# Kernel optimization log

Measured on AMD Instinct MI355X. Metric: run time of the kernel, lower is better.

The kernel has to match this reference:

```python
import jax, jax.numpy as jnp
import numpy as np

NUM_LAYERS = 6
D_MODEL = 256
N_HEADS = 8
N_LEVELS = 4
N_POINTS = 4
D_FFN = 1024
HEAD_DIM = D_MODEL // N_HEADS
B = 2
NQ = 1600
SPATIAL = np.array([[64, 64], [32, 32], [16, 16], [8, 8]], dtype=np.int64)  # (H_l, W_l)
LEVEL_START = np.concatenate([[0], np.cumsum(SPATIAL.prod(1))[:-1]]).astype(np.int64)
S_TOTAL = int(SPATIAL.prod(1).sum())  # 5440


def layer_norm(x, g, b, eps=1e-5):
    mu = x.mean(-1, keepdims=True)
    var = ((x - mu) ** 2).mean(-1, keepdims=True)
    return (x - mu) * jax.lax.rsqrt(var + eps) * g + b


def mha(q, k, v, wq, bq, wk, bk, wv, bv, wo, bo):
    # torch nn.MultiheadAttention math (dropout=eval identity)
    Bb, N, d = q.shape
    def proj(x, w, bias):
        return (x @ w.T + bias).reshape(Bb, -1, N_HEADS, HEAD_DIM).transpose(0, 2, 1, 3)
    qh, kh, vh = proj(q, wq, bq), proj(k, wk, bk), proj(v, wv, bv)
    scores = jnp.einsum('bhqd,bhkd->bhqk', qh, kh) / np.float32(np.sqrt(HEAD_DIM))
    attn = jax.nn.softmax(scores, axis=-1)
    out = jnp.einsum('bhqk,bhkd->bhqd', attn, vh).transpose(0, 2, 1, 3).reshape(Bb, N, d)
    return out @ wo.T + bo


def ms_deform_attn(query, ref_points, src, w_off, b_off, w_attn, b_attn, w_val, b_val, w_out, b_out):
    Bb, Nq, d = query.shape
    value = (src @ w_val.T + b_val).reshape(Bb, -1, N_HEADS, HEAD_DIM)  # [B,S,H,D]
    off = (query @ w_off.T + b_off).reshape(Bb, Nq, N_HEADS, N_LEVELS, N_POINTS, 2)
    aw = (query @ w_attn.T + b_attn).reshape(Bb, Nq, N_HEADS, N_LEVELS * N_POINTS)
    aw = jax.nn.softmax(aw, -1).reshape(Bb, Nq, N_HEADS, N_LEVELS, N_POINTS)
    # offset normalizer is (W_l, H_l)
    norm = jnp.asarray(SPATIAL[:, ::-1].copy(), dtype=query.dtype)  # [L,2]
    loc = ref_points[:, :, None, :, None, :] + off / norm[None, None, None, :, None, :]
    out = jnp.zeros((Bb, Nq, N_HEADS, HEAD_DIM), query.dtype)
    for l in range(N_LEVELS):
        Hl, Wl = int(SPATIAL[l, 0]), int(SPATIAL[l, 1])
        s0 = int(LEVEL_START[l])
        v_l = value[:, s0:s0 + Hl * Wl].transpose(0, 2, 1, 3)  # [B,H,S_l,D]
        loc_l = loc[:, :, :, l]  # [B,Nq,H,P,2]
        # grid_sample bilinear, align_corners=False, padding zeros
        x = loc_l[..., 0] * Wl - 0.5
        y = loc_l[..., 1] * Hl - 0.5
        x0 = jnp.floor(x)
        y0 = jnp.floor(y)
        wx1 = x - x0
        wy1 = y - y0
        samp = jnp.zeros((Bb, Nq, N_HEADS, N_POINTS, HEAD_DIM), query.dtype)
        for dy, wy in ((0, 1.0 - wy1), (1, wy1)):
            for dx, wx in ((0, 1.0 - wx1), (1, wx1)):
                xi = x0 + dx
                yi = y0 + dy
                valid = ((xi >= 0) & (xi <= Wl - 1) & (yi >= 0) & (yi <= Hl - 1)).astype(query.dtype)
                xi_c = jnp.clip(xi, 0, Wl - 1).astype(jnp.int32)
                yi_c = jnp.clip(yi, 0, Hl - 1).astype(jnp.int32)
                idx = (yi_c * Wl + xi_c).transpose(0, 2, 1, 3).reshape(Bb, N_HEADS, Nq * N_POINTS)
                g = jnp.take_along_axis(v_l, idx[..., None], axis=2)  # [B,H,Nq*P,D]
                g = g.reshape(Bb, N_HEADS, Nq, N_POINTS, HEAD_DIM).transpose(0, 2, 1, 3, 4)
                samp = samp + g * (wx * wy * valid)[..., None]
        out = out + (samp * aw[:, :, :, l, :, None]).sum(3)
    return out.reshape(Bb, Nq, d) @ w_out.T + b_out


def decoder_forward(tgt, query_pos, reference_points, src, params):
    out = tgt
    for i in range(NUM_LAYERS):
        p = {k: v[i] for k, v in params.items()}
        q = out + query_pos
        t2 = mha(q, q, out, p['sa_w_q'], p['sa_b_q'], p['sa_w_k'], p['sa_b_k'],
                 p['sa_w_v'], p['sa_b_v'], p['sa_w_o'], p['sa_b_o'])
        out = layer_norm(out + t2, p['ln2_g'], p['ln2_b'])
        t2 = ms_deform_attn(out + query_pos, reference_points, src,
                            p['ca_w_off'], p['ca_b_off'], p['ca_w_attn'], p['ca_b_attn'],
                            p['ca_w_val'], p['ca_b_val'], p['ca_w_out'], p['ca_b_out'])
        out = out + t2
        out = layer_norm(out, p['ln1_g'], p['ln1_b'])
        t2 = jax.nn.relu(out @ p['ffn_w1'].T + p['ffn_b1']) @ p['ffn_w2'].T + p['ffn_b2']
        out = layer_norm(out + t2, p['ln3_g'], p['ln3_b'])
    return out


PARAM_NAMES = ['sa_w_q', 'sa_b_q', 'sa_w_k', 'sa_b_k', 'sa_w_v', 'sa_b_v', 'sa_w_o', 'sa_b_o',
               'ln2_g', 'ln2_b',
               'ca_w_off', 'ca_b_off', 'ca_w_attn', 'ca_b_attn', 'ca_w_val', 'ca_b_val',
               'ca_w_out', 'ca_b_out', 'ln1_g', 'ln1_b',
               'ffn_w1', 'ffn_b1', 'ffn_w2', 'ffn_b2', 'ln3_g', 'ln3_b']


def setup_inputs() -> dict:
    key = jax.random.key(0)
    ks = jax.random.split(key, 64)
    d = D_MODEL
    HLP = N_HEADS * N_LEVELS * N_POINTS
    shapes = {
        'sa_w_q': (d, d), 'sa_b_q': (d,), 'sa_w_k': (d, d), 'sa_b_k': (d,),
        'sa_w_v': (d, d), 'sa_b_v': (d,), 'sa_w_o': (d, d), 'sa_b_o': (d,),
        'ca_w_off': (HLP * 2, d), 'ca_b_off': (HLP * 2,),
        'ca_w_attn': (HLP, d), 'ca_b_attn': (HLP,),
        'ca_w_val': (d, d), 'ca_b_val': (d,),
        'ca_w_out': (d, d), 'ca_b_out': (d,),
        'ffn_w1': (D_FFN, d), 'ffn_b1': (D_FFN,),
        'ffn_w2': (d, D_FFN), 'ffn_b2': (D_FFN * 0 + d,) if False else (d,),
    }
    inp = {}
    inp['tgt'] = jax.random.normal(ks[0], (B, NQ, d), jnp.float32)
    inp['query_pos'] = jax.random.normal(ks[1], (B, NQ, d), jnp.float32)
    inp['reference_points'] = jax.random.uniform(ks[2], (B, NQ, N_LEVELS, 2), jnp.float32)
    inp['src'] = jax.random.normal(ks[3], (B, S_TOTAL, d), jnp.float32)
    i = 4
    for name in PARAM_NAMES:
        if name.startswith('ln'):
            if name.endswith('_g'):
                inp[name] = jnp.ones((NUM_LAYERS, d), jnp.float32)
            else:
                inp[name] = jnp.zeros((NUM_LAYERS, d), jnp.float32)
        else:
            shp = (NUM_LAYERS,) + shapes[name]
            inp[name] = jax.random.normal(ks[i], shp, jnp.float32) * 0.02
            i += 1
    inp['src_spatial_shapes'] = jnp.asarray(SPATIAL)
    inp['src_level_start_index'] = jnp.asarray(LEVEL_START)
    return inp


def reference(tgt, query_pos, reference_points, src,
              sa_w_q, sa_b_q, sa_w_k, sa_b_k, sa_w_v, sa_b_v, sa_w_o, sa_b_o,
              ln2_g, ln2_b,
              ca_w_off, ca_b_off, ca_w_attn, ca_b_attn, ca_w_val, ca_b_val,
              ca_w_out, ca_b_out, ln1_g, ln1_b,
              ffn_w1, ffn_b1, ffn_w2, ffn_b2, ln3_g, ln3_b,
              src_spatial_shapes, src_level_start_index):
    params = dict(zip(PARAM_NAMES, (sa_w_q, sa_b_q, sa_w_k, sa_b_k, sa_w_v, sa_b_v, sa_w_o, sa_b_o,
                                    ln2_g, ln2_b, ca_w_off, ca_b_off, ca_w_attn, ca_b_attn,
                                    ca_w_val, ca_b_val, ca_w_out, ca_b_out, ln1_g, ln1_b,
                                    ffn_w1, ffn_b1, ffn_w2, ffn_b2, ln3_g, ln3_b)))
    return decoder_forward(tgt, query_pos, reference_points, src, params)
```

## Files before the change

kernel.cpp:

```cpp
#include <hip/hip_runtime.h>

#define D_MODEL   256
#define NQ        1600
#define BATCH     2
#define NHEAD     8
#define HDIM      32
#define S_TOTAL   5440
#define D_FFN     1024
#define NUM_LAYERS 6

#define M_Q   (BATCH * NQ)
#define M_V   (BATCH * S_TOTAL)
#define ROW_ELEMS ((size_t)M_Q * D_MODEL)

using short8  = __attribute__((ext_vector_type(8))) short;
using short4v = __attribute__((ext_vector_type(4))) short;
using floatx4 = __attribute__((ext_vector_type(4))) float;

#if __has_builtin(__builtin_amdgcn_mfma_f32_16x16x16_bf16)
  #define MFMA16K16(a,b,c) __builtin_amdgcn_mfma_f32_16x16x16_bf16((a),(b),(c),0,0,0)
#else
  #define MFMA16K16(a,b,c) __builtin_amdgcn_mfma_f32_16x16x16bf16_1k((a),(b),(c),0,0,0)
#endif

#if __has_builtin(__builtin_amdgcn_exp2f)
  #define EXP2F(x) __builtin_amdgcn_exp2f(x)
#else
  #define EXP2F(x) exp2f(x)
#endif

__device__ __forceinline__ ushort f2bf(float f) {
    union { float f; unsigned u; } x; x.f = f;
    unsigned r = (x.u + 0x7fffu + ((x.u >> 16) & 1u)) >> 16;
    return (ushort)r;
}
__device__ __forceinline__ ushort f2bf_trunc(float f) {
    union { float f; unsigned u; } x; x.f = f;
    return (ushort)(x.u >> 16);
}
__device__ __forceinline__ float bf2f(ushort b) {
    union { unsigned u; float f; } x; x.u = ((unsigned)b) << 16;
    return x.f;
}

struct GSeg {
    const ushort* A;
    const ushort* W;
    const float*  bias;
    void*         C;
    int           ldc;
    int           mode;
    int           mblk;
    float         scale;
};
struct GArgs { GSeg s[24]; };

__global__ __launch_bounds__(256) void gemm_multi(GArgs args, int K)
{
    const GSeg sg = args.s[blockIdx.y];
    if ((int)blockIdx.x >= sg.mblk) return;
    __shared__ ushort Al[64][40];
    __shared__ ushort Bl[64][40];
    const int tid  = threadIdx.x;
    const int bm   = blockIdx.x * 64;
    const int lr   = tid >> 2;
    const int lc   = tid & 3;
    const int wave = tid >> 6;
    const int lane = tid & 63;
    const int mo   = (wave & 1) * 32;
    const int no   = (wave >> 1) * 32;
    const int row16 = lane & 15;
    const int quad  = lane >> 4;

    floatx4 acc[2][2] = {};

    const ushort* aG = sg.A + (size_t)(bm + lr) * K + lc * 8;
    const ushort* wG = sg.W + (size_t)lr * K + lc * 8;

    for (int k0 = 0; k0 < K; k0 += 32) {
        __syncthreads();
        *(short8*)&Al[lr][lc * 8] = *(const short8*)(aG + k0);
        *(short8*)&Bl[lr][lc * 8] = *(const short8*)(wG + k0);
        __syncthreads();
        short8 af0 = *(const short8*)&Al[mo + row16][quad * 8];
        short8 af1 = *(const short8*)&Al[mo + 16 + row16][quad * 8];
        short8 bf0 = *(const short8*)&Bl[no + row16][quad * 8];
        short8 bf1 = *(const short8*)&Bl[no + 16 + row16][quad * 8];
        acc[0][0] = __builtin_amdgcn_mfma_f32_16x16x32_bf16(af0, bf0, acc[0][0], 0, 0, 0);
        acc[0][1] = __builtin_amdgcn_mfma_f32_16x16x32_bf16(af0, bf1, acc[0][1], 0, 0, 0);
        acc[1][0] = __builtin_amdgcn_mfma_f32_16x16x32_bf16(af1, bf0, acc[1][0], 0, 0, 0);
        acc[1][1] = __builtin_amdgcn_mfma_f32_16x16x32_bf16(af1, bf1, acc[1][1], 0, 0, 0);
    }

#pragma unroll
    for (int mi = 0; mi < 2; ++mi)
#pragma unroll
        for (int ni = 0; ni < 2; ++ni) {
            const int col = no + ni * 16 + row16;
            const float bv = sg.bias[col];
            const int rowb = bm + mo + mi * 16 + quad * 4;
            if (sg.mode == 4) {
                const int b = rowb / NQ;
                const int mloc = rowb - b * NQ;
                ushort* base = (ushort*)sg.C
                    + ((size_t)b * 8 * NQ + (size_t)(col >> 5) * NQ) * 32 + (col & 31);
#pragma unroll
                for (int r = 0; r < 4; ++r)
                    base[(size_t)(mloc + r) * 32] = f2bf((acc[mi][ni][r] + bv) * sg.scale);
            } else if (sg.mode == 5) {
                const int b = rowb / NQ;
                const int mloc = rowb - b * NQ;
                ushort4 st;
                st.x = f2bf((acc[mi][ni][0] + bv) * sg.scale);
                st.y = f2bf((acc[mi][ni][1] + bv) * sg.scale);
                st.z = f2bf((acc[mi][ni][2] + bv) * sg.scale);
                st.w = f2bf((acc[mi][ni][3] + bv) * sg.scale);
                ushort* base = (ushort*)sg.C
                    + ((size_t)b * 8 * NQ + (size_t)(col >> 5) * NQ) * 32;
                *(ushort4*)(base + ((size_t)(mloc >> 2) * 32 + (col & 31)) * 4) = st;
            } else {
#pragma unroll
                for (int r = 0; r < 4; ++r) {
                    const int row = rowb + r;
                    float v = (acc[mi][ni][r] + bv) * sg.scale;
                    if (sg.mode == 0)
                        ((float*)sg.C)[(size_t)row * sg.ldc + col] = v;
                    else if (sg.mode == 1)
                        ((ushort*)sg.C)[(size_t)row * sg.ldc + col] = f2bf(fmaxf(v, 0.f));
                    else
                        ((ushort*)sg.C)[(size_t)row * sg.ldc + col] = f2bf(v);
                }
            }
        }
}

#define FSHIFT 16.0f

__global__ __launch_bounds__(256) void attn_mfma(const ushort* __restrict__ Qh,
                                                 const ushort* __restrict__ Kh,
                                                 const ushort* __restrict__ Vt,
                                                 ushort* __restrict__ Oh)
{
    const int bh = blockIdx.x;
    const int h  = bh & 7, b = bh >> 3;
    const int q0 = blockIdx.y * 32;
    const int tid  = threadIdx.x;
    const int wave = tid >> 6, lane = tid & 63;
    const int lr   = lane & 15, quad = lane >> 4;

    __shared__ float Ol[4][32][33];
    __shared__ float Ll[4][32];

    const ushort* Qb = Qh + (size_t)bh * NQ * 32;
    const ushort* Kb = Kh + (size_t)bh * NQ * 32;
    const ushort* Vb = Vt + (size_t)bh * NQ * 32;

    const short8 qfA = *(const short8*)(Qb + (size_t)(q0 + lr) * 32 + quad * 8);
    const short8 qfB = *(const short8*)(Qb + (size_t)(q0 + 16 + lr) * 32 + quad * 8);

    float lsumA = 0.f, lsumB = 0.f;
    floatx4 accOA[2] = {}, accOB[2] = {};
    const floatx4 zero = {0.f, 0.f, 0.f, 0.f};

    const int NT = NQ / 64;
    for (int t = wave; t < NT; t += 4) {
        const int k0 = t * 64;
#pragma unroll
        for (int cb = 0; cb < 4; ++cb) {
            const short8 kf = *(const short8*)(Kb + (size_t)(k0 + cb * 16 + lr) * 32 + quad * 8);
            const floatx4 stA = __builtin_amdgcn_mfma_f32_16x16x32_bf16(kf, qfA, zero, 0, 0, 0);
            const floatx4 stB = __builtin_amdgcn_mfma_f32_16x16x32_bf16(kf, qfB, zero, 0, 0, 0);
            const short4v v0 = *(const short4v*)(Vb + (size_t)(k0 + cb * 16 + quad * 4) * 32 + lr * 4);
            const short4v v1 = *(const short4v*)(Vb + (size_t)(k0 + cb * 16 + quad * 4) * 32 + 64 + lr * 4);
            short4v pfA, pfB;
#pragma unroll
            for (int r = 0; r < 4; ++r) {
                const float pA = EXP2F(fminf(stA[r], 100.f) - FSHIFT);
                const float pB = EXP2F(fminf(stB[r], 100.f) - FSHIFT);
                lsumA += pA; lsumB += pB;
                pfA[r] = (short)f2bf_trunc(pA);
                pfB[r] = (short)f2bf_trunc(pB);
            }
            accOA[0] = MFMA16K16(pfA, v0, accOA[0]);
            accOA[1] = MFMA16K16(pfA, v1, accOA[1]);
            accOB[0] = MFMA16K16(pfB, v0, accOB[0]);
            accOB[1] = MFMA16K16(pfB, v1, accOB[1]);
        }
    }

    lsumA += __shfl_xor(lsumA, 16);  lsumB += __shfl_xor(lsumB, 16);
    lsumA += __shfl_xor(lsumA, 32);  lsumB += __shfl_xor(lsumB, 32);
    if (quad == 0) { Ll[wave][lr] = lsumA; Ll[wave][16 + lr] = lsumB; }
#pragma unroll
    for (int r = 0; r < 4; ++r) {
        const int q = quad * 4 + r;
        Ol[wave][q][lr]           = accOA[0][r];
        Ol[wave][q][16 + lr]      = accOA[1][r];
        Ol[wave][16 + q][lr]      = accOB[0][r];
        Ol[wave][16 + q][16 + lr] = accOB[1][r];
    }
    __syncthreads();

#pragma unroll
    for (int i = 0; i < 4; ++i) {
        const int idx = tid + i * 256;
        const int q = idx >> 5, d = idx & 31;
        const float o  = Ol[0][q][d] + Ol[1][q][d] + Ol[2][q][d] + Ol[3][q][d];
        const float lt = Ll[0][q] + Ll[1][q] + Ll[2][q] + Ll[3][q];
        Oh[(size_t)(b * NQ + q0 + q) * 256 + h * 32 + d] = f2bf(o / lt);
    }
}

struct CvtSeg { const float* in; ushort* out; int n4; };
struct CvtArgs { CvtSeg seg[11]; };

__global__ __launch_bounds__(256) void convert_kernel(CvtArgs args)
{
    const CvtSeg sg = args.seg[blockIdx.y];
    const int i = blockIdx.x * 256 + threadIdx.x;
    if (i < sg.n4) {
        float4 v = ((const float4*)sg.in)[i];
        ushort4 o;
        o.x = f2bf(v.x); o.y = f2bf(v.y); o.z = f2bf(v.z); o.w = f2bf(v.w);
        ((ushort4*)sg.out)[i] = o;
    }
}

__global__ __launch_bounds__(256) void init_out_kernel(const float* __restrict__ tgt,
                                                       const float* __restrict__ qpos,
                                                       float* __restrict__ out,
                                                       ushort* __restrict__ out_h,
                                                       ushort* __restrict__ qadd_h, int n4)
{
    const int i = blockIdx.x * 256 + threadIdx.x;
    if (i < n4) {
        float4 v = ((const float4*)tgt)[i];
        float4 p = ((const float4*)qpos)[i];
        ((float4*)out)[i] = v;
        ushort4 o, qa;
        o.x = f2bf(v.x); o.y = f2bf(v.y); o.z = f2bf(v.z); o.w = f2bf(v.w);
        qa.x = f2bf(v.x + p.x); qa.y = f2bf(v.y + p.y);
        qa.z = f2bf(v.z + p.z); qa.w = f2bf(v.w + p.w);
        ((ushort4*)out_h)[i] = o;
        ((ushort4*)qadd_h)[i] = qa;
    }
}

__global__ __launch_bounds__(256) void residual_ln_kernel(const float* __restrict__ x,
                                                          const float* __restrict__ t2,
                                                          const float* __restrict__ g,
                                                          const float* __restrict__ bt,
                                                          const float* __restrict__ qpos,
                                                          float* __restrict__ outp,
                                                          ushort* __restrict__ outp_h,
                                                          ushort* __restrict__ qadd_h)
{
    const int row = blockIdx.x;
    const int c = threadIdx.x;
    const size_t idx = (size_t)row * D_MODEL + c;
    float v = x[idx] + t2[idx];

    float s = v, s2 = v * v;
#pragma unroll
    for (int off = 32; off; off >>= 1) {
        s  += __shfl_xor(s,  off);
        s2 += __shfl_xor(s2, off);
    }
    __shared__ float ws[4], ws2[4];
    const int wid = c >> 6;
    if ((c & 63) == 0) { ws[wid] = s; ws2[wid] = s2; }
    __syncthreads();
    const float tot  = ws[0] + ws[1] + ws[2] + ws[3];
    const float tot2 = ws2[0] + ws2[1] + ws2[2] + ws2[3];
    const float mu  = tot * (1.f / 256.f);
    const float var = tot2 * (1.f / 256.f) - mu * mu;
    const float r = (v - mu) * rsqrtf(var + 1e-5f) * g[c] + bt[c];
    outp[idx] = r;
    outp_h[idx] = f2bf(r);
    qadd_h[idx] = f2bf(r + qpos[idx]);
}

__global__ __launch_bounds__(256) void sample_kernel(const ushort* __restrict__ value,
                                                     const float* __restrict__ off,
                                                     const float* __restrict__ aw,
                                                     const float* __restrict__ ref,
                                                     ushort* __restrict__ outp_h)
{
    const int bq = blockIdx.x;
    const int b  = bq / NQ;
    const int h  = threadIdx.x >> 5;
    const int c  = threadIdx.x & 31;

    const float* offrow = off + (size_t)bq * 256 + h * 32;
    const float* awrow  = aw  + (size_t)bq * 128 + h * 16;
    const float* refrow = ref + (size_t)bq * 8;

    float w16[16];
    {
        float mx = -1e30f;
#pragma unroll
        for (int i = 0; i < 16; ++i) { w16[i] = awrow[i]; mx = fmaxf(mx, w16[i]); }
        float sum = 0.f;
#pragma unroll
        for (int i = 0; i < 16; ++i) { w16[i] = __expf(w16[i] - mx); sum += w16[i]; }
        const float inv = 1.f / sum;
#pragma unroll
        for (int i = 0; i < 16; ++i) w16[i] *= inv;
    }

    const int HL[4]  = {64, 32, 16, 8};
    const int WLv[4] = {64, 32, 16, 8};
    const int S0[4]  = {0, 4096, 5120, 5376};

    float acc = 0.f;
#pragma unroll
    for (int l = 0; l < 4; ++l) {
        const int Hl = HL[l], Wl = WLv[l];
        const float rx = refrow[l * 2 + 0];
        const float ry = refrow[l * 2 + 1];
        const size_t lvl_base = ((size_t)b * S_TOTAL + S0[l]);
#pragma unroll
        for (int p = 0; p < 4; ++p) {
            const float ox = offrow[l * 8 + p * 2 + 0];
            const float oy = offrow[l * 8 + p * 2 + 1];
            const float w  = w16[l * 4 + p];
            const float locx = rx + ox / (float)Wl;
            const float locy = ry + oy / (float)Hl;
            const float x = locx * (float)Wl - 0.5f;
            const float y = locy * (float)Hl - 0.5f;
            const float x0f = floorf(x), y0f = floorf(y);
            const float wx1 = x - x0f, wy1 = y - y0f;
            const int x0 = (int)x0f, y0 = (int)y0f;
#pragma unroll
            for (int dy = 0; dy < 2; ++dy) {
                const int yi = y0 + dy;
                const float wy = dy ? wy1 : (1.f - wy1);
                const bool vy = (yi >= 0) && (yi <= Hl - 1);
                const int yc = min(max(yi, 0), Hl - 1);
#pragma unroll
                for (int dx = 0; dx < 2; ++dx) {
                    const int xi = x0 + dx;
                    const float wx = dx ? wx1 : (1.f - wx1);
                    const bool vx = (xi >= 0) && (xi <= Wl - 1);
                    const int xc = min(max(xi, 0), Wl - 1);
                    const float gv = bf2f(value[((lvl_base + (size_t)yc * Wl + xc)) * 256 + h * 32 + c]);
                    acc += (vx && vy) ? gv * (wx * wy * w) : 0.f;
                }
            }
        }
    }
    outp_h[(size_t)bq * D_MODEL + h * 32 + c] = f2bf(acc);
}

extern "C" void kernel_launch(void* const* d_in, const int* in_sizes, int n_in,
                              void* d_out, int out_size, void* d_ws, size_t ws_size,
                              hipStream_t stream)
{
    const float* tgt  = (const float*)d_in[0];
    const float* qpos = (const float*)d_in[1];
    const float* refp = (const float*)d_in[2];
    const float* src  = (const float*)d_in[3];

    float* bufT   = (float*)d_ws;
    float* bufOff = bufT   + ROW_ELEMS;
    float* bufAw  = bufOff + ROW_ELEMS;

    ushort* out_h   = (ushort*)(bufAw + (size_t)M_Q * 128);
    ushort* qadd_h  = out_h   + ROW_ELEMS;
    ushort* bufX_h  = qadd_h  + ROW_ELEMS;
    ushort* bufQh   = bufX_h  + ROW_ELEMS;
    ushort* bufKh   = bufQh   + ROW_ELEMS;
    ushort* bufVt   = bufKh   + ROW_ELEMS;
    ushort* bufF_h  = bufVt   + ROW_ELEMS;
    ushort* bufVal  = bufF_h  + (size_t)M_Q * D_FFN;
    ushort* src_h   = bufVal  + (size_t)NUM_LAYERS * M_V * D_MODEL;
    ushort* wpool   = src_h   + (size_t)M_V * D_MODEL;

    ushort* wq_h    = wpool;
    ushort* wk_h    = wq_h    + 393216;
    ushort* wv_h    = wk_h    + 393216;
    ushort* wo_h    = wv_h    + 393216;
    ushort* woff_h  = wo_h    + 393216;
    ushort* wattn_h = woff_h  + 393216;
    ushort* wval_h  = wattn_h + 196608;
    ushort* wout_h  = wval_h  + 393216;
    ushort* w1_h    = wout_h  + 393216;
    ushort* w2_h    = w1_h    + 1572864;

    float* out = (float*)d_out;

    CvtArgs ca;
    ca.seg[0]  = { src,                    src_h,   (int)((size_t)M_V * D_MODEL / 4) };
    ca.seg[1]  = { (const float*)d_in[4],  wq_h,    393216 / 4 };
    ca.seg[2]  = { (const float*)d_in[6],  wk_h,    393216 / 4 };
    ca.seg[3]  = { (const float*)d_in[8],  wv_h,    393216 / 4 };
    ca.seg[4]  = { (const float*)d_in[10], wo_h,    393216 / 4 };
    ca.seg[5]  = { (const float*)d_in[14], woff_h,  393216 / 4 };
    ca.seg[6]  = { (const float*)d_in[16], wattn_h, 196608 / 4 };
    ca.seg[7]  = { (const float*)d_in[18], wval_h,  393216 / 4 };
    ca.seg[8]  = { (const float*)d_in[20], wout_h,  393216 / 4 };
    ca.seg[9]  = { (const float*)d_in[24], w1_h,    1572864 / 4 };
    ca.seg[10] = { (const float*)d_in[26], w2_h,    1572864 / 4 };
    convert_kernel<<<dim3(2720, 11), 256, 0, stream>>>(ca);

    init_out_kernel<<<800, 256, 0, stream>>>(tgt, qpos, out, out_h, qadd_h, (int)(ROW_ELEMS / 4));

    const float QSCALE = 0.1767766952966369f * 1.4426950408889634f;
    const int MB_Q = M_Q / 64;
    const int MB_V = M_V / 64;

    {
        GArgs gv;
        for (int l = 0; l < NUM_LAYERS; ++l) {
            const ushort* wl = wval_h + (size_t)l * 65536;
            const float* bv  = (const float*)d_in[19] + (size_t)l * 256;
            ushort* dst = bufVal + (size_t)l * M_V * D_MODEL;
            for (int i = 0; i < 4; ++i)
                gv.s[l * 4 + i] = { src_h, wl + (size_t)i * 64 * 256, bv + i * 64,
                                    dst + i * 64, 256, 2, MB_V, 1.f };
        }
        gemm_multi<<<dim3(MB_V, 24), 256, 0, stream>>>(gv, 256);
    }

    for (int l = 0; l < NUM_LAYERS; ++l) {
        const float* sa_b_q    = (const float*)d_in[5]  + (size_t)l * 256;
        const float* sa_b_k    = (const float*)d_in[7]  + (size_t)l * 256;
        const float* sa_b_v    = (const float*)d_in[9]  + (size_t)l * 256;
        const float* sa_b_o    = (const float*)d_in[11] + (size_t)l * 256;
        const float* ln2_g     = (const float*)d_in[12] + (size_t)l * 256;
        const float* ln2_b     = (const float*)d_in[13] + (size_t)l * 256;
        const float* ca_b_off  = (const float*)d_in[15] + (size_t)l * 256;
        const float* ca_b_attn = (const float*)d_in[17] + (size_t)l * 128;
        const float* ca_b_out  = (const float*)d_in[21] + (size_t)l * 256;
        const float* ln1_g     = (const float*)d_in[22] + (size_t)l * 256;
        const float* ln1_b     = (const float*)d_in[23] + (size_t)l * 256;
        const float* ffn_b1    = (const float*)d_in[25] + (size_t)l * 1024;
        const float* ffn_b2    = (const float*)d_in[27] + (size_t)l * 256;
        const float* ln3_g     = (const float*)d_in[28] + (size_t)l * 256;
        const float* ln3_b     = (const float*)d_in[29] + (size_t)l * 256;

        const ushort* wq = wq_h    + (size_t)l * 65536;
        const ushort* wk = wk_h    + (size_t)l * 65536;
        const ushort* wv = wv_h    + (size_t)l * 65536;
        const ushort* wo = wo_h    + (size_t)l * 65536;
        const ushort* wf = woff_h  + (size_t)l * 65536;
        const ushort* wa = wattn_h + (size_t)l * 32768;
        const ushort* wu = wout_h  + (size_t)l * 65536;
        const ushort* w1 = w1_h    + (size_t)l * 262144;
        const ushort* w2 = w2_h    + (size_t)l * 262144;

        ushort* valL = bufVal + (size_t)l * M_V * D_MODEL;

        GArgs ga;

        for (int i = 0; i < 4; ++i) {
            ga.s[i]     = { qadd_h, wq + (size_t)i * 64 * 256, sa_b_q + i * 64,
                            bufQh + (size_t)(2 * i) * NQ * 32, 0, 4, MB_Q, QSCALE };
            ga.s[4 + i] = { qadd_h, wk + (size_t)i * 64 * 256, sa_b_k + i * 64,
                            bufKh + (size_t)(2 * i) * NQ * 32, 0, 4, MB_Q, 1.f };
            ga.s[8 + i] = { out_h,  wv + (size_t)i * 64 * 256, sa_b_v + i * 64,
                            bufVt + (size_t)(2 * i) * NQ * 32, 0, 5, MB_Q, 1.f };
        }
        gemm_multi<<<dim3(MB_Q, 12), 256, 0, stream>>>(ga, 256);

        attn_mfma<<<dim3(16, NQ / 32), 256, 0, stream>>>(bufQh, bufKh, bufVt, bufX_h);

        for (int i = 0; i < 4; ++i)
            ga.s[i] = { bufX_h, wo + (size_t)i * 64 * 256, sa_b_o + i * 64, bufT + i * 64, 256, 0, MB_Q, 1.f };
        gemm_multi<<<dim3(MB_Q, 4), 256, 0, stream>>>(ga, 256);

        residual_ln_kernel<<<M_Q, 256, 0, stream>>>(out, bufT, ln2_g, ln2_b, qpos, out, out_h, qadd_h);

        for (int i = 0; i < 4; ++i)
            ga.s[i] = { qadd_h, wf + (size_t)i * 64 * 256, ca_b_off + i * 64, bufOff + i * 64, 256, 0, MB_Q, 1.f };
        for (int i = 0; i < 2; ++i)
            ga.s[4 + i] = { qadd_h, wa + (size_t)i * 64 * 256, ca_b_attn + i * 64, bufAw + i * 64, 128, 0, MB_Q, 1.f };
        gemm_multi<<<dim3(MB_Q, 6), 256, 0, stream>>>(ga, 256);

        sample_kernel<<<M_Q, 256, 0, stream>>>(valL, bufOff, bufAw, refp, bufX_h);

        for (int i = 0; i < 4; ++i)
            ga.s[i] = { bufX_h, wu + (size_t)i * 64 * 256, ca_b_out + i * 64, bufT + i * 64, 256, 0, MB_Q, 1.f };
        gemm_multi<<<dim3(MB_Q, 4), 256, 0, stream>>>(ga, 256);

        residual_ln_kernel<<<M_Q, 256, 0, stream>>>(out, bufT, ln1_g, ln1_b, qpos, out, out_h, qadd_h);

        for (int i = 0; i < 16; ++i)
            ga.s[i] = { out_h, w1 + (size_t)i * 64 * 256, ffn_b1 + i * 64, bufF_h + i * 64, 1024, 1, MB_Q, 1.f };
        gemm_multi<<<dim3(MB_Q, 16), 256, 0, stream>>>(ga, 256);

        for (int i = 0; i < 4; ++i)
            ga.s[i] = { bufF_h, w2 + (size_t)i * 64 * 1024, ffn_b2 + i * 64, bufT + i * 64, 256, 0, MB_Q, 1.f };
        gemm_multi<<<dim3(MB_Q, 4), 256, 0, stream>>>(ga, 1024);

        residual_ln_kernel<<<M_Q, 256, 0, stream>>>(out, bufT, ln3_g, ln3_b, qpos, out, out_h, qadd_h);
    }

    (void)in_sizes; (void)n_in; (void)out_size; (void)ws_size;
}
```

Before: 873.8 us.

## Fuse output projection GEMMs with residual add and LayerNorm

Adds a gemm_ln kernel in which each block computes a full 16-row by 256-column tile of the projection (out-proj, cross-attn out, FFN2). It then adds bias and residual, computes LayerNorm in-register with shuffles and shared-memory reductions, and writes the fp32, bf16 and query-pos-added outputs. This removes the intermediate bufT round trip and three separate LN launches per layer. The trade-off is small 16-row tiles that reload the whole weight matrix per block with no double buffering, only 200 blocks, and use of the 16x16x32 MFMA.

```diff
diff --git a/kernel.cpp b/kernel.cpp
--- a/kernel.cpp
+++ b/kernel.cpp
@@ -134,6 +134,95 @@
         }
 }
 
+__global__ __launch_bounds__(256) void gemm_ln(const ushort* __restrict__ A,
+                                               const ushort* __restrict__ W,
+                                               const float* __restrict__ bias,
+                                               const float* __restrict__ g,
+                                               const float* __restrict__ bt,
+                                               const float* __restrict__ qpos,
+                                               const float* __restrict__ resid,
+                                               float* __restrict__ outp,
+                                               ushort* __restrict__ outp_h,
+                                               ushort* __restrict__ qadd_h,
+                                               int K)
+{
+    __shared__ ushort St[272][40];
+    __shared__ float  R1[4][16], R2[4][16];
+    const int tid  = threadIdx.x;
+    const int bm   = blockIdx.x * 16;
+    const int wave = tid >> 6, lane = tid & 63;
+    const int lr   = lane & 15, quad = lane >> 4;
+
+    floatx4 acc[4] = {};
+
+    for (int k0 = 0; k0 < K; k0 += 32) {
+        __syncthreads();
+#pragma unroll
+        for (int i = 0; i < 5; ++i) {
+            const int c = tid + i * 256;
+            if (c < 272 * 4) {
+                const int row = c >> 2, kc = c & 3;
+                const ushort* src = (row < 16)
+                    ? (A + (size_t)(bm + row) * K + k0 + kc * 8)
+                    : (W + (size_t)(row - 16) * K + k0 + kc * 8);
+                *(short8*)&St[row][kc * 8] = *(const short8*)src;
+            }
+        }
+        __syncthreads();
+        const short8 af = *(const short8*)&St[lr][quad * 8];
+#pragma unroll
+        for (int ng = 0; ng < 4; ++ng) {
+            const short8 bf = *(const short8*)&St[16 + wave * 64 + ng * 16 + lr][quad * 8];
+            acc[ng] = __builtin_amdgcn_mfma_f32_16x16x32_bf16(af, bf, acc[ng], 0, 0, 0);
+        }
+    }
+
+#pragma unroll
+    for (int ng = 0; ng < 4; ++ng) {
+        const int col = wave * 64 + ng * 16 + lr;
+        const float bv = bias[col];
+#pragma unroll
+        for (int r = 0; r < 4; ++r)
+            acc[ng][r] += bv + resid[(size_t)(bm + quad * 4 + r) * 256 + col];
+    }
+
+#pragma unroll
+    for (int r = 0; r < 4; ++r) {
+        float s1 = acc[0][r] + acc[1][r] + acc[2][r] + acc[3][r];
+        float s2 = acc[0][r]*acc[0][r] + acc[1][r]*acc[1][r]
+                 + acc[2][r]*acc[2][r] + acc[3][r]*acc[3][r];
+        s1 += __shfl_xor(s1, 1); s2 += __shfl_xor(s2, 1);
+        s1 += __shfl_xor(s1, 2); s2 += __shfl_xor(s2, 2);
+        s1 += __shfl_xor(s1, 4); s2 += __shfl_xor(s2, 4);
+        s1 += __shfl_xor(s1, 8); s2 += __shfl_xor(s2, 8);
+        if (lr == 0) {
+            R1[wave][quad * 4 + r] = s1;
+            R2[wave][quad * 4 + r] = s2;
+        }
+    }
+    __syncthreads();
+
+#pragma unroll
+    for (int r = 0; r < 4; ++r) {
+        const int rl = quad * 4 + r;
+        const float tot1 = R1[0][rl] + R1[1][rl] + R1[2][rl] + R1[3][rl];
+        const float tot2 = R2[0][rl] + R2[1][rl] + R2[2][rl] + R2[3][rl];
+        const float mu  = tot1 * (1.f / 256.f);
+        const float var = tot2 * (1.f / 256.f) - mu * mu;
+        const float rs  = rsqrtf(var + 1e-5f);
+        const int row = bm + rl;
+#pragma unroll
+        for (int ng = 0; ng < 4; ++ng) {
+            const int col = wave * 64 + ng * 16 + lr;
+            const size_t idx = (size_t)row * 256 + col;
+            const float rv = (acc[ng][r] - mu) * rs * g[col] + bt[col];
+            outp[idx]   = rv;
+            outp_h[idx] = f2bf(rv);
+            qadd_h[idx] = f2bf(rv + qpos[idx]);
+        }
+    }
+}
+
 #define FSHIFT 16.0f
 
 __global__ __launch_bounds__(256) void attn_mfma(const ushort* __restrict__ Qh,
@@ -246,40 +335,6 @@
     }
 }
 
-__global__ __launch_bounds__(256) void residual_ln_kernel(const float* __restrict__ x,
-                                                          const float* __restrict__ t2,
-                                                          const float* __restrict__ g,
-                                                          const float* __restrict__ bt,
-                                                          const float* __restrict__ qpos,
-                                                          float* __restrict__ outp,
-                                                          ushort* __restrict__ outp_h,
-                                                          ushort* __restrict__ qadd_h)
-{
-    const int row = blockIdx.x;
-    const int c = threadIdx.x;
-    const size_t idx = (size_t)row * D_MODEL + c;
-    float v = x[idx] + t2[idx];
-
-    float s = v, s2 = v * v;
-#pragma unroll
-    for (int off = 32; off; off >>= 1) {
-        s  += __shfl_xor(s,  off);
-        s2 += __shfl_xor(s2, off);
-    }
-    __shared__ float ws[4], ws2[4];
-    const int wid = c >> 6;
-    if ((c & 63) == 0) { ws[wid] = s; ws2[wid] = s2; }
-    __syncthreads();
-    const float tot  = ws[0] + ws[1] + ws[2] + ws[3];
-    const float tot2 = ws2[0] + ws2[1] + ws2[2] + ws2[3];
-    const float mu  = tot * (1.f / 256.f);
-    const float var = tot2 * (1.f / 256.f) - mu * mu;
-    const float r = (v - mu) * rsqrtf(var + 1e-5f) * g[c] + bt[c];
-    outp[idx] = r;
-    outp_h[idx] = f2bf(r);
-    qadd_h[idx] = f2bf(r + qpos[idx]);
-}
-
 __global__ __launch_bounds__(256) void sample_kernel(const ushort* __restrict__ value,
                                                      const float* __restrict__ off,
                                                      const float* __restrict__ aw,
@@ -361,8 +416,7 @@
     const float* refp = (const float*)d_in[2];
     const float* src  = (const float*)d_in[3];
 
-    float* bufT   = (float*)d_ws;
-    float* bufOff = bufT   + ROW_ELEMS;
+    float* bufOff = (float*)d_ws;
     float* bufAw  = bufOff + ROW_ELEMS;
 
     ushort* out_h   = (ushort*)(bufAw + (size_t)M_Q * 128);
@@ -408,6 +462,7 @@
     const float QSCALE = 0.1767766952966369f * 1.4426950408889634f;
     const int MB_Q = M_Q / 64;
     const int MB_V = M_V / 64;
+    const int LB_Q = M_Q / 16;
 
     {
         GArgs gv;
@@ -465,11 +520,8 @@
 
         attn_mfma<<<dim3(16, NQ / 32), 256, 0, stream>>>(bufQh, bufKh, bufVt, bufX_h);
 
-        for (int i = 0; i < 4; ++i)
-            ga.s[i] = { bufX_h, wo + (size_t)i * 64 * 256, sa_b_o + i * 64, bufT + i * 64, 256, 0, MB_Q, 1.f };
-        gemm_multi<<<dim3(MB_Q, 4), 256, 0, stream>>>(ga, 256);
-
-        residual_ln_kernel<<<M_Q, 256, 0, stream>>>(out, bufT, ln2_g, ln2_b, qpos, out, out_h, qadd_h);
+        gemm_ln<<<LB_Q, 256, 0, stream>>>(bufX_h, wo, sa_b_o, ln2_g, ln2_b, qpos,
+                                          out, out, out_h, qadd_h, 256);
 
         for (int i = 0; i < 4; ++i)
             ga.s[i] = { qadd_h, wf + (size_t)i * 64 * 256, ca_b_off + i * 64, bufOff + i * 64, 256, 0, MB_Q, 1.f };
@@ -479,21 +531,15 @@
 
         sample_kernel<<<M_Q, 256, 0, stream>>>(valL, bufOff, bufAw, refp, bufX_h);
 
-        for (int i = 0; i < 4; ++i)
-            ga.s[i] = { bufX_h, wu + (size_t)i * 64 * 256, ca_b_out + i * 64, bufT + i * 64, 256, 0, MB_Q, 1.f };
-        gemm_multi<<<dim3(MB_Q, 4), 256, 0, stream>>>(ga, 256);
-
-        residual_ln_kernel<<<M_Q, 256, 0, stream>>>(out, bufT, ln1_g, ln1_b, qpos, out, out_h, qadd_h);
+        gemm_ln<<<LB_Q, 256, 0, stream>>>(bufX_h, wu, ca_b_out, ln1_g, ln1_b, qpos,
+                                          out, out, out_h, qadd_h, 256);
 
         for (int i = 0; i < 16; ++i)
             ga.s[i] = { out_h, w1 + (size_t)i * 64 * 256, ffn_b1 + i * 64, bufF_h + i * 64, 1024, 1, MB_Q, 1.f };
         gemm_multi<<<dim3(MB_Q, 16), 256, 0, stream>>>(ga, 256);
 
-        for (int i = 0; i < 4; ++i)
-            ga.s[i] = { bufF_h, w2 + (size_t)i * 64 * 1024, ffn_b2 + i * 64, bufT + i * 64, 256, 0, MB_Q, 1.f };
-        gemm_multi<<<dim3(MB_Q, 4), 256, 0, stream>>>(ga, 1024);
-
-        residual_ln_kernel<<<M_Q, 256, 0, stream>>>(out, bufT, ln3_g, ln3_b, qpos, out, out_h, qadd_h);
+        gemm_ln<<<LB_Q, 256, 0, stream>>>(bufF_h, w2, ffn_b2, ln3_g, ln3_b, qpos,
+                                          out, out, out_h, qadd_h, 1024);
     }
 
     (void)in_sizes; (void)n_in; (void)out_size; (void)ws_size;
```

Result: slower. 1.014 ms (+16.1%).
